# Optimization experiments

Hardware: AMD Instinct MI355X
Metric: run time of the kernel (lower is better)

The kernel has to match this reference:

```python
import jax, jax.numpy as jnp
import numpy as np

BN_EPS = 1e-5

def conv3x3(x, w, b):
    # x: (B,C,H,W), w: (O,C,3,3) -> (B,O,H,W), padding=1 == SAME for 3x3 stride 1
    y = jax.lax.conv_general_dilated(x, w, window_strides=(1, 1), padding='SAME',
                                     dimension_numbers=('NCHW', 'OIHW', 'NCHW'))
    return y + b[None, :, None, None]

def batchnorm(x, gamma, beta):
    # training-mode BatchNorm2d: per-channel batch stats over (N,H,W), biased variance
    mean = jnp.mean(x, axis=(0, 2, 3), keepdims=True)
    var = jnp.var(x, axis=(0, 2, 3), keepdims=True)
    return (x - mean) * jax.lax.rsqrt(var + BN_EPS) * gamma[None, :, None, None] + beta[None, :, None, None]


def setup_inputs() -> dict:
    key = jax.random.key(0)
    ks = jax.random.split(key, 4)
    B, E, T, Fr, H = 16, 16, 1024, 80, 8
    # xavier-ish scale for conv weights
    w_in = jax.random.normal(ks[1], (3 * H, E, 3, 3), jnp.float32) * (1.0 / np.sqrt(E * 9))
    w_out = jax.random.normal(ks[2], (E, 2 * H, 3, 3), jnp.float32) * (1.0 / np.sqrt(2 * H * 9))
    return {
        'x': jax.random.normal(ks[0], (B, E, T, Fr), jnp.float32),
        'w_in': w_in,
        'b_in': jnp.zeros((3 * H,), jnp.float32),
        'w_out': w_out,
        'b_out': jnp.zeros((E,), jnp.float32),
        'gq': jnp.ones((H,), jnp.float32), 'bq': jnp.zeros((H,), jnp.float32),
        'gk': jnp.ones((H,), jnp.float32), 'bk': jnp.zeros((H,), jnp.float32),
        'gv': jnp.ones((H,), jnp.float32), 'bv': jnp.zeros((H,), jnp.float32),
        'go': jnp.ones((E,), jnp.float32), 'bo': jnp.zeros((E,), jnp.float32),
    }


def reference(x, w_in, b_in, w_out, b_out, gq, bq, gk, bk, gv, bv, go, bo):
    B, E, T, Fr = x.shape
    H = w_in.shape[0] // 3
    scaling = E ** (-0.5)  # head_dim == embed_dim in this module

    qkv = conv3x3(x, w_in, b_in)                      # (B, 3H, T, F)
    q, k, v = jnp.split(qkv, 3, axis=1)               # each (B, H, T, F)
    q = q * scaling

    q = jax.nn.relu(batchnorm(q, gq, bq)).reshape(B * H, T, Fr)
    k = jax.nn.relu(batchnorm(k, gk, bk)).reshape(B * H, T, Fr)
    v = jax.nn.relu(batchnorm(v, gv, bv)).reshape(B * H, T, Fr)

    # time-axis attention: (BH,T,F) x (BH,S,F) -> (BH,T,S)
    aw_t = jax.nn.softmax(jnp.einsum('btf,bsf->bts', q, k), axis=-1)
    attn_t = jnp.einsum('bts,bsf->btf', aw_t, v)      # (BH, T, F)

    # freq-axis attention: q^T @ k -> (BH,F,F); then @ v^T -> (BH,F,T)
    aw_f = jax.nn.softmax(jnp.einsum('btf,btg->bfg', q, k), axis=-1)
    attn_f = jnp.einsum('bfg,btg->bft', aw_f, v)      # (BH, F, T)

    attn_t = attn_t.reshape(B, H, T, Fr)
    attn_f = attn_f.transpose(0, 2, 1).reshape(B, H, T, Fr)
    attn = jnp.concatenate([attn_t, attn_f], axis=1)  # (B, 2H, T, F)

    out = jax.nn.relu(batchnorm(conv3x3(attn, w_out, b_out), go, bo))  # (B, E, T, F)
    aw_t_avg = aw_t.reshape(B, H, T, T).sum(axis=1) / H                # (B, T, T)
    return out, aw_t_avg
```

## Files before the change

### kernel.cpp

```cpp
#include <hip/hip_runtime.h>
#include <cstdint>
#include <cstddef>

#define NB 16
#define NT 1024
#define NF 80
#define NH 8
#define FP 96
#define FS 84
#define SP 1032
#define KP 108
#define VP 264

typedef _Float16 v8h __attribute__((ext_vector_type(8)));
typedef _Float16 v4h __attribute__((ext_vector_type(4)));
typedef _Float16 v2h __attribute__((ext_vector_type(2)));
typedef float v4f __attribute__((ext_vector_type(4)));

static const size_t OUT_ELEMS = (size_t)NB * 16 * NT * NF;

__global__ __launch_bounds__(256) void cl_k(const float* __restrict__ src,
                                            _Float16* __restrict__ dst) {
  const int b = blockIdx.y, t0 = blockIdx.x * 16;
  for (int i = threadIdx.x; i < 16 * FS; i += 256) {
    int lt = i / FS, s = i % FS;
    int t = t0 + lt, f = s - 1;
    v8h lo = (v8h)(_Float16)0.f, hi = (v8h)(_Float16)0.f;
    if (f >= 0 && f < NF) {
#pragma unroll
      for (int c = 0; c < 8; ++c)
        lo[c] = (_Float16)src[((size_t)(b * 16 + c) * NT + t) * NF + f];
#pragma unroll
      for (int c = 0; c < 8; ++c)
        hi[c] = (_Float16)src[((size_t)(b * 16 + 8 + c) * NT + t) * NF + f];
    }
    _Float16* d = dst + ((size_t)(b * NT + t) * FS + s) * 16;
    *(v8h*)d = lo;
    *(v8h*)(d + 8) = hi;
  }
}

template <int OCT, int OSTRIDE, bool QSCALE, bool PADOUT>
__global__ __launch_bounds__(512) void conv_mfma_k(
    const _Float16* __restrict__ xcl, const float* __restrict__ w,
    const float* __restrict__ bias, _Float16* __restrict__ out,
    float* __restrict__ pstats, int CO) {
  __shared__ _Float16 axt[18][FS * 16];
  __shared__ _Float16 wlds[3][2][OCT * 16][32];
  __shared__ float blds[32];
  __shared__ float wsum[8][OCT][16], wsq[8][OCT][16];
  const int b = blockIdx.y, t0 = blockIdx.x * 16;
  const int tid = threadIdx.x;
  const int NW = 3 * 2 * OCT * 16 * 32;
  for (int i = tid; i < NW; i += 512) {
    int kk = i % 32;
    int oc = (i / 32) % (OCT * 16);
    int ck = (i / (32 * OCT * 16)) % 2;
    int kt = i / (64 * OCT * 16);
    int kg = ck * 32 + kk;
    float v = 0.f;
    if (oc < CO && kg < 48) {
      int c = kg & 15, kf = kg >> 4;
      v = w[((oc * 16 + c) * 3 + kt) * 3 + kf];
      if (QSCALE && oc < 8) v *= 0.25f;
    }
    wlds[kt][ck][oc][kk] = (_Float16)v;
  }
  if (tid < 32) {
    float v = (tid < CO) ? bias[tid] : 0.f;
    if (QSCALE && tid < 8) v *= 0.25f;
    blds[tid] = v;
  }
  for (int i = tid; i < 18 * 168; i += 512) {
    int r = i / 168, j = i % 168;
    int t = t0 + r - 1;
    int4 v = {0, 0, 0, 0};
    if (t >= 0 && t < NT)
      v = ((const int4*)(xcl + (size_t)(b * NT + t) * FS * 16))[j];
    ((int4*)axt[r])[j] = v;
  }
  __syncthreads();
  const int wv = tid >> 6, l = tid & 63, lg = l >> 4, lm = l & 15;
  v8h bfr[3][2][OCT];
#pragma unroll
  for (int kt = 0; kt < 3; ++kt)
#pragma unroll
    for (int ck = 0; ck < 2; ++ck)
#pragma unroll
      for (int ot = 0; ot < OCT; ++ot)
        bfr[kt][ck][ot] = *(const v8h*)&wlds[kt][ck][ot * 16 + lm][lg * 8];
  float s1[OCT], s2[OCT];
#pragma unroll
  for (int ot = 0; ot < OCT; ++ot) { s1[ot] = 0.f; s2[ot] = 0.f; }
#pragma unroll
  for (int li = 0; li < 2; ++li) {
    const int lt = wv * 2 + li;
    const int tt = t0 + lt;
#pragma unroll
    for (int f0 = 0; f0 < 80; f0 += 16) {
      v4f acc[OCT];
#pragma unroll
      for (int ot = 0; ot < OCT; ++ot) acc[ot] = (v4f){0.f, 0.f, 0.f, 0.f};
#pragma unroll
      for (int kt = 0; kt < 3; ++kt)
#pragma unroll
        for (int ck = 0; ck < 2; ++ck) {
          v8h afr =
              *(const v8h*)&axt[lt + kt][(f0 + lm) * 16 + ck * 32 + lg * 8];
#pragma unroll
          for (int ot = 0; ot < OCT; ++ot)
            acc[ot] = __builtin_amdgcn_mfma_f32_16x16x32_f16(
                afr, bfr[kt][ck][ot], acc[ot], 0, 0, 0);
        }
#pragma unroll
      for (int ot = 0; ot < OCT; ++ot) {
        int oc = ot * 16 + lm;
        if (oc < CO) {
          float bv = blds[oc];
          v4h o;
#pragma unroll
          for (int r = 0; r < 4; ++r) {
            float v = acc[ot][r] + bv;
            s1[ot] += v;
            s2[ot] += v * v;
            o[r] = (_Float16)v;
          }
          *(v4h*)(out + ((size_t)(b * CO + oc) * NT + tt) * OSTRIDE + f0 +
                  lg * 4) = o;
        }
      }
    }
  }
  if constexpr (PADOUT) {
    for (int i = tid; i < CO * 16 * 2; i += 512) {
      int oc = i / 32, lt2 = (i / 2) % 16, half = i & 1;
      int4 z = {0, 0, 0, 0};
      ((int4*)(out + ((size_t)(b * CO + oc) * NT + t0 + lt2) * OSTRIDE +
               80))[half] = z;
    }
  }
#pragma unroll
  for (int ot = 0; ot < OCT; ++ot) {
    float a = s1[ot], b2 = s2[ot];
    a += __shfl_xor(a, 16);
    a += __shfl_xor(a, 32);
    b2 += __shfl_xor(b2, 16);
    b2 += __shfl_xor(b2, 32);
    if (l < 16) { wsum[wv][ot][lm] = a; wsq[wv][ot][lm] = b2; }
  }
  __syncthreads();
  if (tid < CO) {
    int ot = tid >> 4, lmm = tid & 15;
    float a = 0.f, b2 = 0.f;
#pragma unroll
    for (int w2 = 0; w2 < 8; ++w2) { a += wsum[w2][ot][lmm]; b2 += wsq[w2][ot][lmm]; }
    int bid = blockIdx.y * 64 + blockIdx.x;
    pstats[tid * 1024 + bid] = a;
    pstats[(CO + tid) * 1024 + bid] = b2;
  }
}

__global__ __launch_bounds__(256) void bn_finalize2_k(
    const float* __restrict__ pstats, float* __restrict__ stats, int C) {
  const int c = blockIdx.x;
  float a = 0.f, b2 = 0.f;
  for (int i = threadIdx.x; i < 1024; i += 256) {
    a += pstats[c * 1024 + i];
    b2 += pstats[(C + c) * 1024 + i];
  }
  __shared__ float rs[256], rs2[256];
  rs[threadIdx.x] = a;
  rs2[threadIdx.x] = b2;
  __syncthreads();
  for (int off = 128; off > 0; off >>= 1) {
    if ((int)threadIdx.x < off) {
      rs[threadIdx.x] += rs[threadIdx.x + off];
      rs2[threadIdx.x] += rs2[threadIdx.x + off];
    }
    __syncthreads();
  }
  if (threadIdx.x == 0) {
    const float N = 16.0f * (float)(NT * NF);
    float mean = rs[0] / N;
    float var = rs2[0] / N - mean * mean;
    stats[c * 2 + 0] = mean;
    stats[c * 2 + 1] = rsqrtf(var + 1e-5f);
  }
}

__global__ __launch_bounds__(256) void bn_apply_qkv_k(
    _Float16* __restrict__ qkv, const float* __restrict__ stats,
    const float* __restrict__ gq, const float* __restrict__ bq,
    const float* __restrict__ gk, const float* __restrict__ bk,
    const float* __restrict__ gv, const float* __restrict__ bv) {
  const size_t n8 = (size_t)NB * 24 * NT * 12;
  const size_t stride = (size_t)gridDim.x * blockDim.x;
  for (size_t idx = (size_t)blockIdx.x * blockDim.x + threadIdx.x; idx < n8;
       idx += stride) {
    int fc = (int)(idx % 12);
    if (fc >= 10) continue;
    int c = (int)((idx / (NT * 12)) % 24);
    float g, be;
    if (c < 8) { g = gq[c]; be = bq[c]; }
    else if (c < 16) { g = gk[c - 8]; be = bk[c - 8]; }
    else { g = gv[c - 16]; be = bv[c - 16]; }
    float mean = stats[c * 2 + 0], invstd = stats[c * 2 + 1];
    v8h v = ((v8h*)qkv)[idx];
#pragma unroll
    for (int j = 0; j < 8; ++j) {
      float f = (float)v[j];
      f = fmaxf((f - mean) * invstd * g + be, 0.f);
      v[j] = (_Float16)f;
    }
    ((v8h*)qkv)[idx] = v;
  }
}

__global__ __launch_bounds__(256) void vtrans_k(
    const _Float16* __restrict__ qkv, _Float16* __restrict__ vT) {
  __shared__ _Float16 tile[128 * 100];
  const int tc = blockIdx.x, bh = blockIdx.y;
  const int b = bh >> 3, h = bh & 7;
  const int t0 = tc * 128;
  const _Float16* src = qkv + ((size_t)(b * 24 + 16 + h) * NT + t0) * FP;
  const int tid = threadIdx.x;
  for (int i = tid; i < 1536; i += 256) {
    int row = i / 12, c = i % 12;
    int4 v = ((const int4*)src)[i];
    int2* d = (int2*)&tile[row * 100 + c * 8];
    d[0] = make_int2(v.x, v.y);
    d[1] = make_int2(v.z, v.w);
  }
  __syncthreads();
  _Float16* dst = vT + (size_t)bh * 80 * NT + t0;
  for (int i = tid; i < 1280; i += 256) {
    int f = i / 16, c8 = i % 16;
    v8h v;
#pragma unroll
    for (int j = 0; j < 8; ++j) v[j] = tile[(c8 * 8 + j) * 100 + f];
    *(v8h*)(dst + (size_t)f * NT + c8 * 8) = v;
  }
}

__global__ __launch_bounds__(512) void time_attn_k(
    const _Float16* __restrict__ qkv, const _Float16* __restrict__ vT,
    float* __restrict__ attn_out, float* __restrict__ aw_avg) {
  __shared__ _Float16 s_lds[32 * SP];
  __shared__ _Float16 q_lds[32 * KP];
  __shared__ _Float16 kst[256 * KP];
  __shared__ float inv_lds[32];
  const int b = blockIdx.y, t0 = blockIdx.x * 32;
  const int tid = threadIdx.x;
  const int w = tid >> 6, l = tid & 63, lg = l >> 4, lm = l & 15;
  const int grp = tid >> 5, lane = tid & 31;
  float avg[2][32];
#pragma unroll
  for (int rr = 0; rr < 2; ++rr)
#pragma unroll
    for (int k = 0; k < 32; ++k) avg[rr][k] = 0.f;

  int4 rb[6];
  auto gloadK = [&](const _Float16* base, int chunk) {
    const int4* src = (const int4*)(base + (size_t)chunk * 256 * FP);
#pragma unroll
    for (int u = 0; u < 6; ++u) rb[u] = src[tid + u * 512];
  };
  auto lwriteK = [&]() {
#pragma unroll
    for (int u = 0; u < 6; ++u) {
      int i = tid + u * 512, row = i / 12, j = i % 12;
      int2* d = (int2*)&kst[row * KP + j * 8];
      d[0] = make_int2(rb[u].x, rb[u].y);
      d[1] = make_int2(rb[u].z, rb[u].w);
    }
  };
  auto gloadV = [&](const int4* vt4, int chunk) {
#pragma unroll
    for (int u = 0; u < 5; ++u) {
      int i = tid + u * 512, row = i >> 5, c = i & 31;
      rb[u] = vt4[row * 128 + chunk * 32 + c];
    }
  };
  auto lwriteV = [&]() {
#pragma unroll
    for (int u = 0; u < 5; ++u) {
      int i = tid + u * 512, row = i >> 5, c = i & 31;
      *(int4*)&kst[row * VP + c * 8] = rb[u];
    }
  };

  gloadK(qkv + (size_t)(b * 24 + 8) * NT * FP, 0);

  for (int h = 0; h < NH; ++h) {
    const _Float16* qb = qkv + ((size_t)(b * 24 + h) * NT + t0) * FP;
    const _Float16* kb = qkv + (size_t)(b * 24 + 8 + h) * NT * FP;
    const int4* vt4 = (const int4*)(vT + (size_t)(b * 8 + h) * 80 * NT);
    int4 qreg = {0, 0, 0, 0};
    if (tid < 384) qreg = ((const int4*)qb)[tid];
    lwriteK();
    if (tid < 384) {
      int row = tid / 12, j = tid % 12;
      int2* d = (int2*)&q_lds[row * KP + j * 8];
      d[0] = make_int2(qreg.x, qreg.y);
      d[1] = make_int2(qreg.z, qreg.w);
    }
    gloadK(kb, 1);
    __syncthreads();
    v8h qfr[2][3];
#pragma unroll
    for (int qt = 0; qt < 2; ++qt)
#pragma unroll
      for (int kk = 0; kk < 3; ++kk) {
        v4h a0 = *(const v4h*)&q_lds[(qt * 16 + lm) * KP + kk * 32 + lg * 8];
        v4h a1 =
            *(const v4h*)&q_lds[(qt * 16 + lm) * KP + kk * 32 + lg * 8 + 4];
        qfr[qt][kk] = __builtin_shufflevector(a0, a1, 0, 1, 2, 3, 4, 5, 6, 7);
      }
    v4f accO[2][5];
#pragma unroll
    for (int qt = 0; qt < 2; ++qt)
#pragma unroll
      for (int ft = 0; ft < 5; ++ft) accO[qt][ft] = (v4f){0.f, 0.f, 0.f, 0.f};

    for (int s = 0; s < 8; ++s) {
      if (s == 4) {
#pragma unroll
        for (int rr = 0; rr < 2; ++rr) {
          const int row = grp + rr * 16;
          _Float16* srow = &s_lds[row * SP];
          v2h ev[16];
          float m = -1e30f;
#pragma unroll
          for (int k = 0; k < 16; ++k) {
            ev[k] = *(const v2h*)&srow[lane * 2 + k * 64];
            m = fmaxf(m, fmaxf((float)ev[k][0], (float)ev[k][1]));
          }
#pragma unroll
          for (int mk = 16; mk; mk >>= 1) m = fmaxf(m, __shfl_xor(m, mk, 32));
          float d = 0.f;
#pragma unroll
          for (int k = 0; k < 16; ++k) {
            float e0 = __expf((float)ev[k][0] - m);
            float e1 = __expf((float)ev[k][1] - m);
            d += e0 + e1;
            v2h w2;
            w2[0] = (_Float16)e0;
            w2[1] = (_Float16)e1;
            ev[k] = w2;
            *(v2h*)&srow[lane * 2 + k * 64] = w2;
          }
#pragma unroll
          for (int mk = 16; mk; mk >>= 1) d += __shfl_xor(d, mk, 32);
          float inv = 1.f / d;
          if (lane == 0) inv_lds[row] = inv;
#pragma unroll
          for (int k = 0; k < 16; ++k) {
            avg[rr][2 * k] += (float)ev[k][0] * inv;
            avg[rr][2 * k + 1] += (float)ev[k][1] * inv;
          }
        }
        __syncthreads();
      }
      if (s < 4) {
#pragma unroll
        for (int tt = 0; tt < 2; ++tt) {
          const int rowb = (w * 2 + tt) * 16;
          const int rbase = (rowb + lm) * KP;
          v8h kfr[3];
#pragma unroll
          for (int kk = 0; kk < 3; ++kk) {
            v4h b0 = *(const v4h*)&kst[rbase + kk * 32 + lg * 8];
            v4h b1 = *(const v4h*)&kst[rbase + kk * 32 + lg * 8 + 4];
            kfr[kk] = __builtin_shufflevector(b0, b1, 0, 1, 2, 3, 4, 5, 6, 7);
          }
          const int sc = s * 256 + rowb + lg * 4;
#pragma unroll
          for (int qt = 0; qt < 2; ++qt) {
            v4f acc = (v4f){0.f, 0.f, 0.f, 0.f};
#pragma unroll
            for (int kk = 0; kk < 3; ++kk)
              acc = __builtin_amdgcn_mfma_f32_16x16x32_f16(kfr[kk],
                                                           qfr[qt][kk], acc,
                                                           0, 0, 0);
            v4h o;
#pragma unroll
            for (int r = 0; r < 4; ++r) o[r] = (_Float16)acc[r];
            *(v4h*)&s_lds[(qt * 16 + lm) * SP + sc] = o;
          }
        }
      } else {
        const int vcb = (s - 4) * 256;
        v8h pfr[2];
#pragma unroll
        for (int qt = 0; qt < 2; ++qt)
          pfr[qt] =
              *(const v8h*)&s_lds[(qt * 16 + lm) * SP + vcb + w * 32 + lg * 8];
#pragma unroll
        for (int ft = 0; ft < 5; ++ft) {
          v8h bfr = *(const v8h*)&kst[(ft * 16 + lm) * VP + w * 32 + lg * 8];
          accO[0][ft] = __builtin_amdgcn_mfma_f32_16x16x32_f16(
              pfr[0], bfr, accO[0][ft], 0, 0, 0);
          accO[1][ft] = __builtin_amdgcn_mfma_f32_16x16x32_f16(
              pfr[1], bfr, accO[1][ft], 0, 0, 0);
        }
      }
      __syncthreads();
      if (s < 7) {
        if (s + 1 < 4) lwriteK(); else lwriteV();
        int ns = s + 2;
        if (ns < 4) gloadK(kb, ns);
        else if (ns < 8) gloadV(vt4, ns - 4);
        else if (h < 7)
          gloadK(qkv + (size_t)(b * 24 + 8 + h + 1) * NT * FP, 0);
        __syncthreads();
      }
    }
    float* ored = (float*)s_lds;
#pragma unroll
    for (int qt = 0; qt < 2; ++qt) {
#pragma unroll
      for (int ft = 0; ft < 5; ++ft)
#pragma unroll
        for (int r = 0; r < 4; ++r)
          ored[(w * 16 + lg * 4 + r) * 84 + ft * 16 + lm] =
              accO[qt][ft][r] * inv_lds[qt * 16 + lg * 4 + r];
      __syncthreads();
      for (int i = tid; i < 1280; i += 512) {
        int q = i / 80, f = i % 80;
        float ss = 0.f;
#pragma unroll
        for (int ww = 0; ww < 8; ++ww) ss += ored[(ww * 16 + q) * 84 + f];
        attn_out[((size_t)(b * 16 + h) * NT + t0 + qt * 16 + q) * NF + f] = ss;
      }
      __syncthreads();
    }
  }
#pragma unroll
  for (int rr = 0; rr < 2; ++rr) {
    float* ab = aw_avg + ((size_t)b * NT + t0 + grp + rr * 16) * NT;
#pragma unroll
    for (int k = 0; k < 16; ++k) {
      float2 v2;
      v2.x = avg[rr][2 * k] * 0.125f;
      v2.y = avg[rr][2 * k + 1] * 0.125f;
      *(float2*)&ab[lane * 2 + k * 64] = v2;
    }
  }
}

__global__ __launch_bounds__(64) void freq_qk_k(
    const _Float16* __restrict__ qkv, float* __restrict__ Cp) {
  __shared__ _Float16 qs[128 * 100];
  __shared__ _Float16 ks[128 * 100];
  const int tc = blockIdx.x, bh = blockIdx.y;
  const int b = bh >> 3, h = bh & 7;
  const int t0 = tc * 128;
  const _Float16* qb = qkv + ((size_t)(b * 24 + h) * NT + t0) * FP;
  const _Float16* kb = qkv + ((size_t)(b * 24 + 8 + h) * NT + t0) * FP;
  const int tid = threadIdx.x;
  for (int i = tid; i < 1536; i += 64) {
    int row = i / 12, c = i % 12;
    int4 vq = ((const int4*)qb)[i];
    int4 vk = ((const int4*)kb)[i];
    int2* dq = (int2*)&qs[row * 100 + c * 8];
    dq[0] = make_int2(vq.x, vq.y);
    dq[1] = make_int2(vq.z, vq.w);
    int2* dk = (int2*)&ks[row * 100 + c * 8];
    dk[0] = make_int2(vk.x, vk.y);
    dk[1] = make_int2(vk.z, vk.w);
  }
  __syncthreads();
  const int lg = tid >> 4, lm = tid & 15;
  v4f acc[5][5];
#pragma unroll
  for (int fr = 0; fr < 5; ++fr)
#pragma unroll
    for (int gc = 0; gc < 5; ++gc) acc[fr][gc] = (v4f){0.f, 0.f, 0.f, 0.f};
#pragma unroll
  for (int kk = 0; kk < 4; ++kk) {
    v8h afr[5];
#pragma unroll
    for (int fr = 0; fr < 5; ++fr)
#pragma unroll
      for (int j = 0; j < 8; ++j)
        afr[fr][j] = qs[(kk * 32 + lg * 8 + j) * 100 + fr * 16 + lm];
#pragma unroll
    for (int gc = 0; gc < 5; ++gc) {
      v8h bfr;
#pragma unroll
      for (int j = 0; j < 8; ++j)
        bfr[j] = ks[(kk * 32 + lg * 8 + j) * 100 + gc * 16 + lm];
#pragma unroll
      for (int fr = 0; fr < 5; ++fr)
        acc[fr][gc] = __builtin_amdgcn_mfma_f32_16x16x32_f16(afr[fr], bfr,
                                                             acc[fr][gc], 0,
                                                             0, 0);
    }
  }
  float* cpb = Cp + ((size_t)bh * 8 + tc) * 6400;
#pragma unroll
  for (int fr = 0; fr < 5; ++fr)
#pragma unroll
    for (int gc = 0; gc < 5; ++gc)
#pragma unroll
      for (int r = 0; r < 4; ++r)
        cpb[(fr * 16 + lg * 4 + r) * 80 + gc * 16 + lm] = acc[fr][gc][r];
}

__global__ __launch_bounds__(128) void freq_sm_k(const float* __restrict__ Cp,
                                                 _Float16* __restrict__ P) {
  const int bh = blockIdx.x;
  const int f = threadIdx.x;
  if (f >= 80) return;
  float c[80];
#pragma unroll
  for (int g = 0; g < 80; ++g) c[g] = 0.f;
  const float* base = Cp + (size_t)bh * 8 * 6400 + f * 80;
#pragma unroll
  for (int tc = 0; tc < 8; ++tc) {
    const float4* p4 = (const float4*)(base + tc * 6400);
#pragma unroll
    for (int g4 = 0; g4 < 20; ++g4) {
      float4 v = p4[g4];
      c[g4 * 4 + 0] += v.x;
      c[g4 * 4 + 1] += v.y;
      c[g4 * 4 + 2] += v.z;
      c[g4 * 4 + 3] += v.w;
    }
  }
  float m = -1e30f;
#pragma unroll
  for (int g = 0; g < 80; ++g) m = fmaxf(m, c[g]);
  float d = 0.f;
#pragma unroll
  for (int g = 0; g < 80; ++g) {
    float e = __expf(c[g] - m);
    d += e;
    c[g] = e;
  }
  float inv = 1.f / d;
  _Float16* pb = P + (size_t)bh * 80 * 96 + (size_t)f * 96;
#pragma unroll
  for (int c8 = 0; c8 < 10; ++c8) {
    v8h v;
#pragma unroll
    for (int j = 0; j < 8; ++j) v[j] = (_Float16)(c[c8 * 8 + j] * inv);
    *(v8h*)(pb + c8 * 8) = v;
  }
  v8h z = (v8h)(_Float16)0.f;
  *(v8h*)(pb + 80) = z;
  *(v8h*)(pb + 88) = z;
}

__global__ __launch_bounds__(256) void freq_pv_k(
    const _Float16* __restrict__ qkv, const _Float16* __restrict__ P,
    float* __restrict__ attn_out) {
  __shared__ _Float16 vs[128 * 104];
  __shared__ _Float16 ps[80 * 104];
  const int tc = blockIdx.x, bh = blockIdx.y;
  const int b = bh >> 3, h = bh & 7;
  const int t0 = tc * 128;
  const _Float16* vb = qkv + ((size_t)(b * 24 + 16 + h) * NT + t0) * FP;
  const _Float16* pb = P + (size_t)bh * 80 * 96;
  const int tid = threadIdx.x;
  for (int i = tid; i < 1536; i += 256) {
    int row = i / 12, c = i % 12;
    *(int4*)&vs[row * 104 + c * 8] = ((const int4*)vb)[i];
  }
  for (int i = tid; i < 960; i += 256) {
    int row = i / 12, c = i % 12;
    *(int4*)&ps[row * 104 + c * 8] = ((const int4*)pb)[i];
  }
  __syncthreads();
  const int w = tid >> 6, l = tid & 63, lg = l >> 4, lm = l & 15;
  v8h bfr[5][3];
#pragma unroll
  for (int fc = 0; fc < 5; ++fc)
#pragma unroll
    for (int kk = 0; kk < 3; ++kk)
      bfr[fc][kk] = *(const v8h*)&ps[(fc * 16 + lm) * 104 + kk * 32 + lg * 8];
#pragma unroll
  for (int tt2 = 0; tt2 < 2; ++tt2) {
    const int tt = w + tt2 * 4;
    v8h afr[3];
#pragma unroll
    for (int kk = 0; kk < 3; ++kk)
      afr[kk] = *(const v8h*)&vs[(tt * 16 + lm) * 104 + kk * 32 + lg * 8];
    float* ob =
        attn_out + ((size_t)(b * 16 + 8 + h) * NT + t0 + tt * 16) * NF;
#pragma unroll
    for (int fc = 0; fc < 5; ++fc) {
      v4f acc = (v4f){0.f, 0.f, 0.f, 0.f};
#pragma unroll
      for (int kk = 0; kk < 3; ++kk)
        acc = __builtin_amdgcn_mfma_f32_16x16x32_f16(afr[kk], bfr[fc][kk],
                                                     acc, 0, 0, 0);
#pragma unroll
      for (int r = 0; r < 4; ++r)
        ob[(lg * 4 + r) * NF + fc * 16 + lm] = acc[r];
    }
  }
}

__global__ __launch_bounds__(256) void bn_apply_out_k(
    const _Float16* __restrict__ y, const float* __restrict__ stats,
    const float* __restrict__ go, const float* __restrict__ bo,
    float* __restrict__ out) {
  const size_t n8 = OUT_ELEMS / 8;
  const size_t stride = (size_t)gridDim.x * blockDim.x;
  for (size_t idx = (size_t)blockIdx.x * blockDim.x + threadIdx.x; idx < n8;
       idx += stride) {
    int c = (int)((idx / (NT * NF / 8)) % 16);
    float g = go[c], be = bo[c];
    float mean = stats[c * 2 + 0], invstd = stats[c * 2 + 1];
    v8h v = ((const v8h*)y)[idx];
    float4 o0, o1;
    o0.x = fmaxf(((float)v[0] - mean) * invstd * g + be, 0.f);
    o0.y = fmaxf(((float)v[1] - mean) * invstd * g + be, 0.f);
    o0.z = fmaxf(((float)v[2] - mean) * invstd * g + be, 0.f);
    o0.w = fmaxf(((float)v[3] - mean) * invstd * g + be, 0.f);
    o1.x = fmaxf(((float)v[4] - mean) * invstd * g + be, 0.f);
    o1.y = fmaxf(((float)v[5] - mean) * invstd * g + be, 0.f);
    o1.z = fmaxf(((float)v[6] - mean) * invstd * g + be, 0.f);
    o1.w = fmaxf(((float)v[7] - mean) * invstd * g + be, 0.f);
    ((float4*)out)[idx * 2] = o0;
    ((float4*)out)[idx * 2 + 1] = o1;
  }
}

extern "C" void kernel_launch(void* const* d_in, const int* in_sizes, int n_in,
                              void* d_out, int out_size, void* d_ws,
                              size_t ws_size, hipStream_t stream) {
  const float* x = (const float*)d_in[0];
  const float* w_in = (const float*)d_in[1];
  const float* b_in = (const float*)d_in[2];
  const float* w_out = (const float*)d_in[3];
  const float* b_out = (const float*)d_in[4];
  const float* gq = (const float*)d_in[5];
  const float* bq = (const float*)d_in[6];
  const float* gk = (const float*)d_in[7];
  const float* bk = (const float*)d_in[8];
  const float* gv = (const float*)d_in[9];
  const float* bv = (const float*)d_in[10];
  const float* go = (const float*)d_in[11];
  const float* bo = (const float*)d_in[12];

  float* out = (float*)d_out;
  float* aw = out + OUT_ELEMS;
  char* wsb = (char*)d_ws;
  _Float16* qkvb = (_Float16*)wsb;
  _Float16* yh = (_Float16*)wsb;
  _Float16* xcl = (_Float16*)(wsb + 75497472);
  _Float16* acl = xcl;
  _Float16* vTb = (_Float16*)(wsb + 75497472);
  float* Cp = (float*)(wsb + 75497472);
  _Float16* Pf = (_Float16*)(wsb + 101711872);
  float* pstats = (float*)(wsb + 119537664);
  float* stats1 = pstats + 49152;
  float* stats2 = stats1 + 48;

  cl_k<<<dim3(64, 16), 256, 0, stream>>>(x, xcl);
  conv_mfma_k<2, FP, true, true>
      <<<dim3(64, 16), 512, 0, stream>>>(xcl, w_in, b_in, qkvb, pstats, 24);
  bn_finalize2_k<<<24, 256, 0, stream>>>(pstats, stats1, 24);
  bn_apply_qkv_k<<<2048, 256, 0, stream>>>(qkvb, stats1, gq, bq, gk, bk, gv,
                                           bv);
  vtrans_k<<<dim3(8, 128), 256, 0, stream>>>(qkvb, vTb);
  time_attn_k<<<dim3(32, 16), 512, 0, stream>>>(qkvb, vTb, out, aw);
  freq_qk_k<<<dim3(8, 128), 64, 0, stream>>>(qkvb, Cp);
  freq_sm_k<<<128, 128, 0, stream>>>(Cp, Pf);
  freq_pv_k<<<dim3(8, 128), 256, 0, stream>>>(qkvb, Pf, out);
  cl_k<<<dim3(64, 16), 256, 0, stream>>>(out, acl);
  conv_mfma_k<1, NF, false, false>
      <<<dim3(64, 16), 512, 0, stream>>>(acl, w_out, b_out, yh, pstats, 16);
  bn_finalize2_k<<<16, 256, 0, stream>>>(pstats, stats2, 16);
  bn_apply_out_k<<<2048, 256, 0, stream>>>(yh, stats2, go, bo, out);
}
```

Before: 437.1 us.

## Fuse channel-last conversion into conv loads and BN of V into transpose

Removes the standalone cl_k layout-conversion kernels. Each conv block now reads fp32 NCHW input directly, converts it to fp16 and writes it into its shared-memory tile, zeroing the padding columns itself. This drops the intermediate fp16 buffer round trip and two launches, but conv blocks now re-read overlapping halo rows from fp32 global memory. It also splits the QKV BN apply so Q/K are normalized in place while V's BN+ReLU is fused into the transpose kernel, saving a pass over V.

```diff
diff --git a/kernel.cpp b/kernel.cpp
--- a/kernel.cpp
+++ b/kernel.cpp
@@ -19,30 +19,9 @@
 
 static const size_t OUT_ELEMS = (size_t)NB * 16 * NT * NF;
 
-__global__ __launch_bounds__(256) void cl_k(const float* __restrict__ src,
-                                            _Float16* __restrict__ dst) {
-  const int b = blockIdx.y, t0 = blockIdx.x * 16;
-  for (int i = threadIdx.x; i < 16 * FS; i += 256) {
-    int lt = i / FS, s = i % FS;
-    int t = t0 + lt, f = s - 1;
-    v8h lo = (v8h)(_Float16)0.f, hi = (v8h)(_Float16)0.f;
-    if (f >= 0 && f < NF) {
-#pragma unroll
-      for (int c = 0; c < 8; ++c)
-        lo[c] = (_Float16)src[((size_t)(b * 16 + c) * NT + t) * NF + f];
-#pragma unroll
-      for (int c = 0; c < 8; ++c)
-        hi[c] = (_Float16)src[((size_t)(b * 16 + 8 + c) * NT + t) * NF + f];
-    }
-    _Float16* d = dst + ((size_t)(b * NT + t) * FS + s) * 16;
-    *(v8h*)d = lo;
-    *(v8h*)(d + 8) = hi;
-  }
-}
-
 template <int OCT, int OSTRIDE, bool QSCALE, bool PADOUT>
 __global__ __launch_bounds__(512) void conv_mfma_k(
-    const _Float16* __restrict__ xcl, const float* __restrict__ w,
+    const float* __restrict__ src, const float* __restrict__ w,
     const float* __restrict__ bias, _Float16* __restrict__ out,
     float* __restrict__ pstats, int CO) {
   __shared__ _Float16 axt[18][FS * 16];
@@ -71,13 +50,26 @@
     if (QSCALE && tid < 8) v *= 0.25f;
     blds[tid] = v;
   }
-  for (int i = tid; i < 18 * 168; i += 512) {
-    int r = i / 168, j = i % 168;
+  for (int i = tid; i < 144; i += 512) {
+    int r = i / 8, j = i % 8;
+    int sidx = j >> 1, half = j & 1;
+    int site = (sidx == 0) ? 0 : 80 + sidx;
+    *(v8h*)&axt[r][site * 16 + half * 8] = (v8h)(_Float16)0.f;
+  }
+  for (int i = tid; i < 18 * 80; i += 512) {
+    int r = i / 80, f = i % 80;
     int t = t0 + r - 1;
-    int4 v = {0, 0, 0, 0};
-    if (t >= 0 && t < NT)
-      v = ((const int4*)(xcl + (size_t)(b * NT + t) * FS * 16))[j];
-    ((int4*)axt[r])[j] = v;
+    v8h lo = (v8h)(_Float16)0.f, hi = (v8h)(_Float16)0.f;
+    if (t >= 0 && t < NT) {
+#pragma unroll
+      for (int c = 0; c < 8; ++c)
+        lo[c] = (_Float16)src[((size_t)(b * 16 + c) * NT + t) * NF + f];
+#pragma unroll
+      for (int c = 0; c < 8; ++c)
+        hi[c] = (_Float16)src[((size_t)(b * 16 + 8 + c) * NT + t) * NF + f];
+    }
+    *(v8h*)&axt[r][(f + 1) * 16] = lo;
+    *(v8h*)&axt[r][(f + 1) * 16 + 8] = hi;
   }
   __syncthreads();
   const int wv = tid >> 6, l = tid & 63, lg = l >> 4, lm = l & 15;
@@ -188,48 +180,64 @@
   }
 }
 
-__global__ __launch_bounds__(256) void bn_apply_qkv_k(
+__global__ __launch_bounds__(256) void bn_apply_qk_k(
     _Float16* __restrict__ qkv, const float* __restrict__ stats,
     const float* __restrict__ gq, const float* __restrict__ bq,
-    const float* __restrict__ gk, const float* __restrict__ bk,
-    const float* __restrict__ gv, const float* __restrict__ bv) {
-  const size_t n8 = (size_t)NB * 24 * NT * 12;
+    const float* __restrict__ gk, const float* __restrict__ bk) {
+  const size_t n8 = (size_t)NB * 16 * NT * 12;
   const size_t stride = (size_t)gridDim.x * blockDim.x;
   for (size_t idx = (size_t)blockIdx.x * blockDim.x + threadIdx.x; idx < n8;
        idx += stride) {
     int fc = (int)(idx % 12);
     if (fc >= 10) continue;
-    int c = (int)((idx / (NT * 12)) % 24);
+    int ch = (int)((idx / (NT * 12)) % 16);
+    int b = (int)(idx / (16 * NT * 12));
+    size_t rest = idx % (NT * 12);
+    size_t v8idx = ((size_t)(b * 24 + ch) * NT * 12) + rest;
     float g, be;
-    if (c < 8) { g = gq[c]; be = bq[c]; }
-    else if (c < 16) { g = gk[c - 8]; be = bk[c - 8]; }
-    else { g = gv[c - 16]; be = bv[c - 16]; }
-    float mean = stats[c * 2 + 0], invstd = stats[c * 2 + 1];
-    v8h v = ((v8h*)qkv)[idx];
+    if (ch < 8) { g = gq[ch]; be = bq[ch]; }
+    else { g = gk[ch - 8]; be = bk[ch - 8]; }
+    float mean = stats[ch * 2 + 0], invstd = stats[ch * 2 + 1];
+    v8h v = ((v8h*)qkv)[v8idx];
 #pragma unroll
     for (int j = 0; j < 8; ++j) {
       float f = (float)v[j];
       f = fmaxf((f - mean) * invstd * g + be, 0.f);
       v[j] = (_Float16)f;
     }
-    ((v8h*)qkv)[idx] = v;
-  }
-}
-
-__global__ __launch_bounds__(256) void vtrans_k(
-    const _Float16* __restrict__ qkv, _Float16* __restrict__ vT) {
+    ((v8h*)qkv)[v8idx] = v;
+  }
+}
+
+__global__ __launch_bounds__(256) void vtrans_bn_k(
+    _Float16* __restrict__ qkv, const float* __restrict__ stats,
+    const float* __restrict__ gv, const float* __restrict__ bv,
+    _Float16* __restrict__ vT) {
   __shared__ _Float16 tile[128 * 100];
   const int tc = blockIdx.x, bh = blockIdx.y;
   const int b = bh >> 3, h = bh & 7;
   const int t0 = tc * 128;
-  const _Float16* src = qkv + ((size_t)(b * 24 + 16 + h) * NT + t0) * FP;
+  _Float16* src = qkv + ((size_t)(b * 24 + 16 + h) * NT + t0) * FP;
   const int tid = threadIdx.x;
+  const float mean = stats[(16 + h) * 2 + 0];
+  const float invstd = stats[(16 + h) * 2 + 1];
+  const float g = gv[h], be = bv[h];
   for (int i = tid; i < 1536; i += 256) {
     int row = i / 12, c = i % 12;
-    int4 v = ((const int4*)src)[i];
+    v8h v = *(v8h*)(src + (size_t)row * FP + c * 8);
+    if (c < 10) {
+#pragma unroll
+      for (int j = 0; j < 8; ++j) {
+        float f = (float)v[j];
+        f = fmaxf((f - mean) * invstd * g + be, 0.f);
+        v[j] = (_Float16)f;
+      }
+      *(v8h*)(src + (size_t)row * FP + c * 8) = v;
+    }
     int2* d = (int2*)&tile[row * 100 + c * 8];
-    d[0] = make_int2(v.x, v.y);
-    d[1] = make_int2(v.z, v.w);
+    int4 vi = __builtin_bit_cast(int4, v);
+    d[0] = make_int2(vi.x, vi.y);
+    d[1] = make_int2(vi.z, vi.w);
   }
   __syncthreads();
   _Float16* dst = vT + (size_t)bh * 80 * NT + t0;
@@ -650,8 +658,6 @@
   char* wsb = (char*)d_ws;
   _Float16* qkvb = (_Float16*)wsb;
   _Float16* yh = (_Float16*)wsb;
-  _Float16* xcl = (_Float16*)(wsb + 75497472);
-  _Float16* acl = xcl;
   _Float16* vTb = (_Float16*)(wsb + 75497472);
   float* Cp = (float*)(wsb + 75497472);
   _Float16* Pf = (_Float16*)(wsb + 101711872);
@@ -659,20 +665,17 @@
   float* stats1 = pstats + 49152;
   float* stats2 = stats1 + 48;
 
-  cl_k<<<dim3(64, 16), 256, 0, stream>>>(x, xcl);
   conv_mfma_k<2, FP, true, true>
-      <<<dim3(64, 16), 512, 0, stream>>>(xcl, w_in, b_in, qkvb, pstats, 24);
+      <<<dim3(64, 16), 512, 0, stream>>>(x, w_in, b_in, qkvb, pstats, 24);
   bn_finalize2_k<<<24, 256, 0, stream>>>(pstats, stats1, 24);
-  bn_apply_qkv_k<<<2048, 256, 0, stream>>>(qkvb, stats1, gq, bq, gk, bk, gv,
-                                           bv);
-  vtrans_k<<<dim3(8, 128), 256, 0, stream>>>(qkvb, vTb);
+  bn_apply_qk_k<<<2048, 256, 0, stream>>>(qkvb, stats1, gq, bq, gk, bk);
+  vtrans_bn_k<<<dim3(8, 128), 256, 0, stream>>>(qkvb, stats1, gv, bv, vTb);
   time_attn_k<<<dim3(32, 16), 512, 0, stream>>>(qkvb, vTb, out, aw);
   freq_qk_k<<<dim3(8, 128), 64, 0, stream>>>(qkvb, Cp);
   freq_sm_k<<<128, 128, 0, stream>>>(Cp, Pf);
   freq_pv_k<<<dim3(8, 128), 256, 0, stream>>>(qkvb, Pf, out);
-  cl_k<<<dim3(64, 16), 256, 0, stream>>>(out, acl);
   conv_mfma_k<1, NF, false, false>
-      <<<dim3(64, 16), 512, 0, stream>>>(acl, w_out, b_out, yh, pstats, 16);
+      <<<dim3(64, 16), 512, 0, stream>>>(out, w_out, b_out, yh, pstats, 16);
   bn_finalize2_k<<<16, 256, 0, stream>>>(pstats, stats2, 16);
   bn_apply_out_k<<<2048, 256, 0, stream>>>(yh, stats2, go, bo, out);
 }
```

Measured after the change: 397.4 us. 9.1% less time.
